# Optimization experiments

Hardware: AMD Instinct MI355X
Metric: run time of the kernel (lower is better)

The kernel has to match this reference:

```python
import jax, jax.numpy as jnp
import numpy as np

N, E = 10000, 320000
IN_CH, HID, OUT_CH, HEADS = 128, 64, 40, 8
NEG_SLOPE = 0.2


def gat_conv(x, src, dst, W, a_src, a_dst, bias, heads, C, concat, n_nodes):
    # x: [N, F_in]; W: [F_in, heads*C]; a_src/a_dst: [heads, C]
    h = (x @ W).reshape(n_nodes, heads, C)              # [N,H,C]
    alpha_src = jnp.sum(h * a_src, axis=-1)             # [N,H]
    alpha_dst = jnp.sum(h * a_dst, axis=-1)             # [N,H]
    score = jax.nn.leaky_relu(alpha_src[src] + alpha_dst[dst], NEG_SLOPE)  # [E,H]
    # segment softmax over edges sharing the same destination node
    smax = jax.ops.segment_max(score, dst, num_segments=n_nodes)
    smax = jnp.where(jnp.isfinite(smax), smax, 0.0)
    ex = jnp.exp(score - smax[dst])
    denom = jax.ops.segment_sum(ex, dst, num_segments=n_nodes)
    alpha = ex / (denom[dst] + 1e-16)                   # [E,H]
    msg = h[src] * alpha[:, :, None]                    # [E,H,C]
    out = jax.ops.segment_sum(msg, dst, num_segments=n_nodes)  # [N,H,C]
    out = out.reshape(n_nodes, heads * C) if concat else out.mean(axis=1)
    return out + bias


def setup_inputs() -> dict:
    key = jax.random.key(0)
    ks = jax.random.split(key, 16)
    g = 0.1
    return {
        "x": jax.random.normal(ks[0], (N, IN_CH), jnp.float32),
        "edge_index": jax.random.randint(ks[1], (2, E), 0, N, jnp.int64),
        "W1": jax.random.normal(ks[2], (IN_CH, HID), jnp.float32) * g,
        "b1": jnp.zeros((HID,), jnp.float32),
        "Wc1": jax.random.normal(ks[3], (HID, HEADS * HID), jnp.float32) * g,
        "att_src1": jax.random.normal(ks[4], (HEADS, HID), jnp.float32) * g,
        "att_dst1": jax.random.normal(ks[5], (HEADS, HID), jnp.float32) * g,
        "bc1": jnp.zeros((HEADS * HID,), jnp.float32),
        "Wc2": jax.random.normal(ks[6], (HEADS * HID, HID), jnp.float32) * g,
        "att_src2": jax.random.normal(ks[7], (1, HID), jnp.float32) * g,
        "att_dst2": jax.random.normal(ks[8], (1, HID), jnp.float32) * g,
        "bc2": jnp.zeros((HID,), jnp.float32),
        "W2": jax.random.normal(ks[9], (HID, OUT_CH), jnp.float32) * g,
        "b2": jnp.zeros((OUT_CH,), jnp.float32),
    }


def reference(x, edge_index, W1, b1, Wc1, att_src1, att_dst1, bc1,
              Wc2, att_src2, att_dst2, bc2, W2, b2):
    # add self-loops (PyG GATConv default add_self_loops=True)
    loop = jnp.arange(N, dtype=edge_index.dtype)
    src = jnp.concatenate([edge_index[0], loop])
    dst = jnp.concatenate([edge_index[1], loop])

    h = jax.nn.relu(x @ W1 + b1)                                   # lin0 + relu (dropout off in eval)
    h = jax.nn.elu(gat_conv(h, src, dst, Wc1, att_src1, att_dst1, bc1,
                            HEADS, HID, True, N))                  # conv1, concat heads
    h = gat_conv(h, src, dst, Wc2, att_src2, att_dst2, bc2,
                 1, HID, False, N)                                 # conv2, single head
    return h @ W2 + b2
```

## Files before the change

### kernel.cpp

```cpp
#include <hip/hip_runtime.h>
#include <cstdint>
#include <cstddef>

#define IN_CH 128
#define HID 64
#define HEADS 8
#define OUT_CH 40
#define NEG 0.2f
#define PAD 128
#define KP 136

typedef __attribute__((ext_vector_type(8))) short bf16x8;
typedef __attribute__((ext_vector_type(4))) float f32x4;

#define MFMA(a, b, c) __builtin_amdgcn_mfma_f32_16x16x32_bf16(a, b, c, 0, 0, 0)

__device__ inline unsigned short f2bf(float f) {
    unsigned u = __float_as_uint(f);
    unsigned r = (u + 0x7FFFu + ((u >> 16) & 1u)) >> 16;
    return (unsigned short)r;
}
__device__ inline float bf2f(unsigned short b) {
    return __uint_as_float((unsigned)b << 16);
}
__device__ inline bf16x8 ldb8(const unsigned short* p) {
    return *reinterpret_cast<const bf16x8*>(p);
}


__global__ void k_init(const float* __restrict__ W1,
                       const float* __restrict__ Wc1, const float* __restrict__ Wc2,
                       const float* __restrict__ as1, const float* __restrict__ ad1,
                       int* __restrict__ cursor,
                       unsigned short* __restrict__ W1T,
                       unsigned short* __restrict__ Wc1T, unsigned short* __restrict__ Wc2T,
                       unsigned short* __restrict__ vaT, int N) {
    int i = blockIdx.x * 256 + threadIdx.x;
    if (i < N) { cursor[i] = 0; return; }
    i -= N;
    if (i < 64 * 128) {
        int j = i >> 7, k = i & 127;
        W1T[i] = f2bf(W1[k * 64 + j]);
        return;
    }
    i -= 64 * 128;
    if (i < 512 * 64) {
        int j = i >> 6, k = i & 63;
        Wc1T[i] = f2bf(Wc1[(size_t)k * 512 + j]);
        return;
    }
    i -= 512 * 64;
    if (i < 64 * 512) {
        int j = i >> 9, k = i & 511;
        Wc2T[i] = f2bf(Wc2[(size_t)k * 64 + j]);
        return;
    }
    i -= 64 * 512;
    if (i < 8192) {
        int u = i >> 3, q = i & 7;
        int t = u >> 6, k = u & 63;
        int h = t & 7;
        const float* a = (t < 8) ? as1 : ad1;
        float sum = 0.f;
#pragma unroll
        for (int c2 = q * 8; c2 < q * 8 + 8; ++c2)
            sum += Wc1[(size_t)k * 512 + h * 64 + c2] * a[h * 64 + c2];
        sum += __shfl_xor(sum, 1);
        sum += __shfl_xor(sum, 2);
        sum += __shfl_xor(sum, 4);
        if (q == 0) vaT[t * 64 + k] = f2bf(sum);
    }
}


__global__ __launch_bounds__(256) void k_lin1m(const float* __restrict__ x,
                                               const unsigned short* __restrict__ W1T,
                                               const float* __restrict__ b1,
                                               const unsigned short* __restrict__ vaT,
                                               unsigned short* __restrict__ h0b,
                                               float* __restrict__ asrc, float* __restrict__ adst,
                                               const int* __restrict__ ei, int E, int T,
                                               int* __restrict__ cursor, int* __restrict__ csrc,
                                               int N, int NB) {
    __shared__ unsigned short h0s[16][72];
    if (blockIdx.x >= NB) {
        int e = (blockIdx.x - NB) * 256 + threadIdx.x;
        if (e < T) {
            int s, d;
            if (e < E) { s = ei[e]; d = ei[E + e]; } else { s = d = e - E; }
            int pos = atomicAdd(&cursor[d], 1);
            csrc[(size_t)d * PAD + pos] = s;
        }
        return;
    }
    int w = threadIdx.x >> 6, l = threadIdx.x & 63;
    int m0 = blockIdx.x * 16;
    int c = l & 15, g = l >> 4;
    int xr = m0 + c; if (xr >= N) xr = N - 1;
    bf16x8 af[4];
    const float* arow = x + (size_t)xr * 128 + 8 * g;
#pragma unroll
    for (int ks = 0; ks < 4; ++ks) {
        float4 f0 = *(const float4*)(arow + 32 * ks);
        float4 f1 = *(const float4*)(arow + 32 * ks + 4);
        bf16x8 t;
        t[0] = (short)f2bf(f0.x); t[1] = (short)f2bf(f0.y);
        t[2] = (short)f2bf(f0.z); t[3] = (short)f2bf(f0.w);
        t[4] = (short)f2bf(f1.x); t[5] = (short)f2bf(f1.y);
        t[6] = (short)f2bf(f1.z); t[7] = (short)f2bf(f1.w);
        af[ks] = t;
    }
    const unsigned short* brow = W1T + (size_t)(16 * w + c) * 128 + 8 * g;
    f32x4 acca = {}, accb = {};
    acca = MFMA(af[0], ldb8(brow), acca);
    accb = MFMA(af[1], ldb8(brow + 32), accb);
    acca = MFMA(af[2], ldb8(brow + 64), acca);
    accb = MFMA(af[3], ldb8(brow + 96), accb);
    f32x4 acc = acca + accb;
    int j = 16 * w + c;
    float bj = b1[j];
#pragma unroll
    for (int r = 0; r < 4; ++r) {
        float v = fmaxf(acc[r] + bj, 0.f);
        unsigned short us = f2bf(v);
        int row = m0 + 4 * g + r;
        if (row < N) h0b[(size_t)row * 64 + j] = us;
        h0s[4 * g + r][j] = us;
    }
    __syncthreads();
    if (w == 0) {
        bf16x8 a0 = ldb8(&h0s[c][8 * g]);
        bf16x8 a1 = ldb8(&h0s[c][32 + 8 * g]);
        bf16x8 b0 = ldb8(&vaT[c * 64 + 8 * g]);
        bf16x8 b1v = ldb8(&vaT[c * 64 + 32 + 8 * g]);
        f32x4 al = {};
        al = MFMA(a0, b0, al);
        al = MFMA(a1, b1v, al);
#pragma unroll
        for (int r = 0; r < 4; ++r) {
            int n = m0 + 4 * g + r;
            if (n < N) {
                if (c < 8) asrc[n * 8 + c] = al[r];
                else       adst[n * 8 + (c - 8)] = al[r];
            }
        }
    }
}


__global__ __launch_bounds__(128) void k_conv1agg(const unsigned short* __restrict__ h0b,
                                                  const float* __restrict__ asrc, const float* __restrict__ adst,
                                                  const int* __restrict__ degs, const int* __restrict__ csrc,
                                                  unsigned short* __restrict__ aggb, int N) {
    __shared__ int srcb[PAD];
    __shared__ float mx[8], den[8], adl[8];
    __shared__ unsigned short wA[16][KP];
    __shared__ unsigned short BT[64][KP];
    float (*sbf)[8] = (float(*)[8]) & BT[0][0];
    int tid = threadIdx.x;
    int n = blockIdx.x;
    int deg = degs[n];
    int K32 = (deg + 31) & ~31;
    if (tid < 8) adl[tid] = adst[n * 8 + tid];
    __syncthreads();
    if (tid < deg) {
        int s = csrc[(size_t)n * PAD + tid];
        srcb[tid] = s;
        const float4* ap = (const float4*)&asrc[(size_t)s * 8];
        float4 a0 = ap[0], a1 = ap[1];
        float v;
        float4 s0, s1;
        v = a0.x + adl[0]; s0.x = (v >= 0.f) ? v : NEG * v;
        v = a0.y + adl[1]; s0.y = (v >= 0.f) ? v : NEG * v;
        v = a0.z + adl[2]; s0.z = (v >= 0.f) ? v : NEG * v;
        v = a0.w + adl[3]; s0.w = (v >= 0.f) ? v : NEG * v;
        v = a1.x + adl[4]; s1.x = (v >= 0.f) ? v : NEG * v;
        v = a1.y + adl[5]; s1.y = (v >= 0.f) ? v : NEG * v;
        v = a1.z + adl[6]; s1.z = (v >= 0.f) ? v : NEG * v;
        v = a1.w + adl[7]; s1.w = (v >= 0.f) ? v : NEG * v;
        *(float4*)&sbf[tid][0] = s0;
        *(float4*)&sbf[tid][4] = s1;
    }
    __syncthreads();
    if (tid < 64) {
        int hh = tid & 7, idx = tid >> 3;
        float m = -1e30f;
        for (int i = idx; i < deg; i += 8) m = fmaxf(m, sbf[i][hh]);
        m = fmaxf(m, __shfl_xor(m, 8));
        m = fmaxf(m, __shfl_xor(m, 16));
        m = fmaxf(m, __shfl_xor(m, 32));
        if (tid < 8) mx[tid] = m;
    }
    __syncthreads();
    if (tid < 64) {
        int hh = tid & 7, idx = tid >> 3;
        float mh = mx[hh];
        float d = 0.f;
        for (int i = idx; i < K32; i += 8) {
            float ev = 0.f;
            if (i < deg) { ev = __expf(sbf[i][hh] - mh); d += ev; }
            wA[hh][i] = f2bf(ev);
        }
        d += __shfl_xor(d, 8);
        d += __shfl_xor(d, 16);
        d += __shfl_xor(d, 32);
        if (tid < 8) den[tid] = d + 1e-16f;
    }
    __syncthreads();
    for (int idx = tid; idx < K32 * 32; idx += 128) {
        int e = idx >> 5, cp = idx & 31;
        unsigned u = 0;
        if (e < deg) u = *(const unsigned*)&h0b[(size_t)srcb[e] * 64 + 2 * cp];
        BT[2 * cp][e] = (unsigned short)(u & 0xFFFFu);
        BT[2 * cp + 1][e] = (unsigned short)(u >> 16);
    }
    __syncthreads();
    int w = tid >> 6, l = tid & 63;
    int c = l & 15, g = l >> 4;
    f32x4 acc0 = {}, acc1 = {};
    for (int ks = 0; ks < (K32 >> 5); ++ks) {
        bf16x8 af = ldb8(&wA[c][32 * ks + 8 * g]);
        acc0 = MFMA(af, ldb8(&BT[32 * w + c][32 * ks + 8 * g]), acc0);
        acc1 = MFMA(af, ldb8(&BT[32 * w + 16 + c][32 * ks + 8 * g]), acc1);
    }
    if (g < 2) {
#pragma unroll
        for (int r = 0; r < 4; ++r) {
            int h = 4 * g + r;
            float dh = den[h];
            aggb[(size_t)n * 512 + h * 64 + 32 * w + c]      = f2bf(acc0[r] / dh);
            aggb[(size_t)n * 512 + h * 64 + 32 * w + 16 + c] = f2bf(acc1[r] / dh);
        }
    }
}


__global__ __launch_bounds__(256) void k_p1l2(const unsigned short* __restrict__ aggb,
                                              const unsigned short* __restrict__ Wc1T,
                                              const float* __restrict__ bc1,
                                              const unsigned short* __restrict__ Wc2T,
                                              const float* __restrict__ as2, const float* __restrict__ ad2,
                                              unsigned short* __restrict__ hc2b,
                                              float* __restrict__ asrc, float* __restrict__ adst, int N) {
    __shared__ unsigned short h1s[16][520];
    __shared__ float pps[4][16][2];
    int w = threadIdx.x >> 6, l = threadIdx.x & 63;
    int m0 = blockIdx.x * 16;
    int c = l & 15, g = l >> 4;
#pragma unroll
    for (int hl = 0; hl < 2; ++hl) {
        int h = 2 * w + hl;
        const unsigned short* arow = aggb + (size_t)(m0 + c) * 512 + h * 64 + 8 * g;
        bf16x8 af0 = ldb8(arow), af1 = ldb8(arow + 32);
        f32x4 acc[4] = {};
#pragma unroll
        for (int nt = 0; nt < 4; ++nt) {
            const unsigned short* brow = Wc1T + (size_t)(h * 64 + 16 * nt + c) * 64 + 8 * g;
            acc[nt] = MFMA(af0, ldb8(brow), acc[nt]);
            acc[nt] = MFMA(af1, ldb8(brow + 32), acc[nt]);
        }
#pragma unroll
        for (int nt = 0; nt < 4; ++nt) {
            int j = h * 64 + 16 * nt + c;
            float bj = bc1[j];
#pragma unroll
            for (int r = 0; r < 4; ++r) {
                float v = acc[nt][r] + bj;
                v = (v > 0.f) ? v : __expf(v) - 1.f;
                h1s[4 * g + r][j] = f2bf(v);
            }
        }
    }
    __syncthreads();
    const unsigned short* brow2 = Wc2T + (size_t)(16 * w + c) * 512 + 8 * g;
    f32x4 acc2a = {}, acc2b = {};
#pragma unroll
    for (int ks = 0; ks < 8; ++ks) {
        acc2a = MFMA(ldb8(&h1s[c][32 * ks + 8 * g]), ldb8(brow2 + 32 * ks), acc2a);
        acc2b = MFMA(ldb8(&h1s[c][32 * (ks + 8) + 8 * g]), ldb8(brow2 + 32 * (ks + 8)), acc2b);
    }
    f32x4 acc2 = acc2a + acc2b;
    int j = 16 * w + c;
    float aj = as2[j], dj = ad2[j];
    float ps[4], pd[4];
#pragma unroll
    for (int r = 0; r < 4; ++r) {
        float v = acc2[r];
        hc2b[(size_t)(m0 + 4 * g + r) * 64 + j] = f2bf(v);
        ps[r] = v * aj;
        pd[r] = v * dj;
    }
#pragma unroll
    for (int r = 0; r < 4; ++r) {
        float s = ps[r], d = pd[r];
        s += __shfl_xor(s, 1); s += __shfl_xor(s, 2); s += __shfl_xor(s, 4); s += __shfl_xor(s, 8);
        d += __shfl_xor(d, 1); d += __shfl_xor(d, 2); d += __shfl_xor(d, 4); d += __shfl_xor(d, 8);
        if (c == 0) {
            pps[w][4 * g + r][0] = s;
            pps[w][4 * g + r][1] = d;
        }
    }
    __syncthreads();
    int tid = threadIdx.x;
    if (tid < 32) {
        int row = tid >> 1, sel = tid & 1;
        float sum = pps[0][row][sel] + pps[1][row][sel] + pps[2][row][sel] + pps[3][row][sel];
        int n = m0 + row;
        if (n < N) {
            if (sel == 0) asrc[n] = sum;
            else          adst[n] = sum;
        }
    }
}


__global__ __launch_bounds__(256) void k_conv2f(const unsigned short* __restrict__ hc2b,
                                                const float* __restrict__ asrc, const float* __restrict__ adst,
                                                const int* __restrict__ degs, const int* __restrict__ csrc,
                                                const float* __restrict__ bc2,
                                                const float* __restrict__ W2, const float* __restrict__ b2,
                                                float* __restrict__ out, int N) {
    __shared__ float w2s[HID * OUT_CH];
    __shared__ float cosh_[4][HID];
    int tid = threadIdx.x;
    for (int i = tid; i < HID * OUT_CH; i += 256) w2s[i] = W2[i];
    int lane = tid & 63, nl = tid >> 6;
    int half = lane >> 5, cl = lane & 31;
    int n = blockIdx.x * 4 + nl;
    if (n < N) {
        int deg = degs[n];
        float ad = adst[n];
        float rm = -1e30f, rden = 0.f;
        float ax = 0.f, ay = 0.f;
        for (int base = 0; base < deg; base += 64) {
            int cnt = min(64, deg - base);
            int s = 0;
            float sc = -1e30f;
            if (lane < cnt) {
                s = csrc[(size_t)n * PAD + base + lane];
                float v = asrc[s] + ad;
                sc = (v >= 0.f) ? v : NEG * v;
            }
            float m = sc;
#pragma unroll
            for (int mm = 1; mm < 64; mm <<= 1) m = fmaxf(m, __shfl_xor(m, mm));
            float nmv = fmaxf(rm, m);
            float scale = __expf(rm - nmv);
            float p = (lane < cnt) ? __expf(sc - nmv) : 0.f;
            float d = p;
#pragma unroll
            for (int mm = 1; mm < 64; mm <<= 1) d += __shfl_xor(d, mm);
            rden = rden * scale + d;
            rm = nmv;
            ax *= scale; ay *= scale;
            for (int i = 0; i < cnt; i += 2) {
                int idx = i + half;
                float pi = __shfl(p, idx);
                int si = __shfl(s, idx);
                unsigned uu = *(const unsigned*)&hc2b[(size_t)si * 64 + 2 * cl];
                ax += pi * bf2f((unsigned short)(uu & 0xFFFFu));
                ay += pi * bf2f((unsigned short)(uu >> 16));
            }
        }
        ax += __shfl_xor(ax, 32);
        ay += __shfl_xor(ay, 32);
        if (half == 0) {
            float inv = 1.f / (rden + 1e-16f);
            cosh_[nl][2 * cl] = ax * inv + bc2[2 * cl];
            cosh_[nl][2 * cl + 1] = ay * inv + bc2[2 * cl + 1];
        }
    }
    __syncthreads();
    if (tid >= 160) return;
    int nn = tid / 40, j = tid % 40;
    int no = blockIdx.x * 4 + nn;
    if (no >= N) return;
    float s = b2[j];
#pragma unroll 8
    for (int k = 0; k < HID; ++k) s += cosh_[nn][k] * w2s[k * OUT_CH + j];
    out[(size_t)no * OUT_CH + j] = s;
}


extern "C" void kernel_launch(void* const* d_in, const int* in_sizes, int n_in,
                              void* d_out, int out_size, void* d_ws, size_t ws_size,
                              hipStream_t stream) {
    const float* x   = (const float*)d_in[0];
    const int*   ei  = (const int*)d_in[1];
    const float* W1  = (const float*)d_in[2];
    const float* b1  = (const float*)d_in[3];
    const float* Wc1 = (const float*)d_in[4];
    const float* as1 = (const float*)d_in[5];
    const float* ad1 = (const float*)d_in[6];
    const float* bc1 = (const float*)d_in[7];
    const float* Wc2 = (const float*)d_in[8];
    const float* as2 = (const float*)d_in[9];
    const float* ad2 = (const float*)d_in[10];
    const float* bc2 = (const float*)d_in[11];
    const float* W2  = (const float*)d_in[12];
    const float* b2  = (const float*)d_in[13];

    const int N = in_sizes[0] / IN_CH;
    const int E = in_sizes[1] / 2;
    const int T = E + N;

    char* base = (char*)d_ws;
    size_t off = 0;
    auto carve = [&](size_t bytes) -> void* {
        off = (off + 255) & ~(size_t)255;
        void* r = base + off;
        off += bytes;
        return r;
    };
    int* cursor     = (int*)carve((size_t)N * 4);
    int* csrc       = (int*)carve((size_t)N * PAD * 4);
    unsigned short* W1T  = (unsigned short*)carve((size_t)64 * 128 * 2);
    unsigned short* Wc1T = (unsigned short*)carve((size_t)512 * 64 * 2);
    unsigned short* Wc2T = (unsigned short*)carve((size_t)64 * 512 * 2);
    unsigned short* vaT  = (unsigned short*)carve((size_t)16 * 64 * 2);
    unsigned short* h0b  = (unsigned short*)carve((size_t)N * 64 * 2);
    float* asrc1    = (float*)carve((size_t)N * 8 * 4);
    float* adst1    = (float*)carve((size_t)N * 8 * 4);
    unsigned short* aggb = (unsigned short*)carve((size_t)N * 512 * 2);
    unsigned short* hc2b = (unsigned short*)carve((size_t)N * 64 * 2);
    float* asrc2    = (float*)carve((size_t)N * 4);
    float* adst2    = (float*)carve((size_t)N * 4);

    int init_total = N + 64 * 128 + 512 * 64 + 64 * 512 + 8192;
    k_init<<<(init_total + 255) / 256, 256, 0, stream>>>(W1, Wc1, Wc2, as1, ad1, cursor,
                                                         W1T, Wc1T, Wc2T, vaT, N);

    int NB = (N + 15) / 16;
    int FB = (T + 255) / 256;
    k_lin1m<<<NB + FB, 256, 0, stream>>>(x, W1T, b1, vaT, h0b, asrc1, adst1,
                                         ei, E, T, cursor, csrc, N, NB);
    k_conv1agg<<<N, 128, 0, stream>>>(h0b, asrc1, adst1, cursor, csrc, aggb, N);
    k_p1l2<<<(N + 15) / 16, 256, 0, stream>>>(aggb, Wc1T, bc1, Wc2T, as2, ad2,
                                              hc2b, asrc2, adst2, N);
    k_conv2f<<<(N + 3) / 4, 256, 0, stream>>>(hc2b, asrc2, adst2, cursor, csrc, bc2, W2, b2,
                                              (float*)d_out, N);
}
```

Before: 111.5 us.

## Rewrite conv1 aggregation as one wavefront per node with online softmax

The conv1 aggregation kernel now assigns one 64-lane wavefront per destination node, eight nodes per 512-thread block, instead of one 128-thread block per node. It replaces the block-wide barriers and the MFMA over a transposed LDS tile with wave-local syncs and scalar FMA accumulation, and uses an online (running max and rescale) softmax over 64-edge chunks. The aim is to cut barrier overhead, per-block launch cost and LDS transpose traffic, and to raise occupancy. In exchange it gives up MFMA throughput, relies on wave-level memory ordering, and issues per-edge 16-bit gathers for each lane.

```diff
diff --git a/kernel.cpp b/kernel.cpp
--- a/kernel.cpp
+++ b/kernel.cpp
@@ -8,7 +8,6 @@
 #define OUT_CH 40
 #define NEG 0.2f
 #define PAD 128
-#define KP 136
 
 typedef __attribute__((ext_vector_type(8))) short bf16x8;
 typedef __attribute__((ext_vector_type(4))) float f32x4;
@@ -25,6 +24,11 @@
 }
 __device__ inline bf16x8 ldb8(const unsigned short* p) {
     return *reinterpret_cast<const bf16x8*>(p);
+}
+__device__ __forceinline__ void wsync() {
+    __builtin_amdgcn_wave_barrier();
+    __threadfence_block();
+    __builtin_amdgcn_wave_barrier();
 }
 
 
@@ -148,90 +152,93 @@
 }
 
 
-__global__ __launch_bounds__(128) void k_conv1agg(const unsigned short* __restrict__ h0b,
+__global__ __launch_bounds__(512) void k_conv1agg(const unsigned short* __restrict__ h0b,
                                                   const float* __restrict__ asrc, const float* __restrict__ adst,
                                                   const int* __restrict__ degs, const int* __restrict__ csrc,
                                                   unsigned short* __restrict__ aggb, int N) {
-    __shared__ int srcb[PAD];
-    __shared__ float mx[8], den[8], adl[8];
-    __shared__ unsigned short wA[16][KP];
-    __shared__ unsigned short BT[64][KP];
-    float (*sbf)[8] = (float(*)[8]) & BT[0][0];
-    int tid = threadIdx.x;
-    int n = blockIdx.x;
+    __shared__ float sbw[8][64][8];
+    __shared__ int srcw[8][64];
+    __shared__ float scl[8][8];
+    __shared__ float dnw[8][8];
+    int w = threadIdx.x >> 6, l = threadIdx.x & 63;
+    int n = blockIdx.x * 8 + w;
+    if (n >= N) return;
     int deg = degs[n];
-    int K32 = (deg + 31) & ~31;
-    if (tid < 8) adl[tid] = adst[n * 8 + tid];
-    __syncthreads();
-    if (tid < deg) {
-        int s = csrc[(size_t)n * PAD + tid];
-        srcb[tid] = s;
-        const float4* ap = (const float4*)&asrc[(size_t)s * 8];
-        float4 a0 = ap[0], a1 = ap[1];
-        float v;
-        float4 s0, s1;
-        v = a0.x + adl[0]; s0.x = (v >= 0.f) ? v : NEG * v;
-        v = a0.y + adl[1]; s0.y = (v >= 0.f) ? v : NEG * v;
-        v = a0.z + adl[2]; s0.z = (v >= 0.f) ? v : NEG * v;
-        v = a0.w + adl[3]; s0.w = (v >= 0.f) ? v : NEG * v;
-        v = a1.x + adl[4]; s1.x = (v >= 0.f) ? v : NEG * v;
-        v = a1.y + adl[5]; s1.y = (v >= 0.f) ? v : NEG * v;
-        v = a1.z + adl[6]; s1.z = (v >= 0.f) ? v : NEG * v;
-        v = a1.w + adl[7]; s1.w = (v >= 0.f) ? v : NEG * v;
-        *(float4*)&sbf[tid][0] = s0;
-        *(float4*)&sbf[tid][4] = s1;
-    }
-    __syncthreads();
-    if (tid < 64) {
-        int hh = tid & 7, idx = tid >> 3;
+    float4 ad0 = *(const float4*)&adst[(size_t)n * 8];
+    float4 ad1 = *(const float4*)&adst[(size_t)n * 8 + 4];
+    int hh = l & 7, idx = l >> 3;
+    float rm = -1e30f, rden = 0.f;
+    float acc[8] = {0.f, 0.f, 0.f, 0.f, 0.f, 0.f, 0.f, 0.f};
+    for (int base = 0; base < deg; base += 64) {
+        int cnt = min(64, deg - base);
+        wsync();
+        if (l < cnt) {
+            int s = csrc[(size_t)n * PAD + base + l];
+            srcw[w][l] = s;
+            float4 a0 = *(const float4*)&asrc[(size_t)s * 8];
+            float4 a1 = *(const float4*)&asrc[(size_t)s * 8 + 4];
+            float v;
+            float4 s0, s1;
+            v = a0.x + ad0.x; s0.x = (v >= 0.f) ? v : NEG * v;
+            v = a0.y + ad0.y; s0.y = (v >= 0.f) ? v : NEG * v;
+            v = a0.z + ad0.z; s0.z = (v >= 0.f) ? v : NEG * v;
+            v = a0.w + ad0.w; s0.w = (v >= 0.f) ? v : NEG * v;
+            v = a1.x + ad1.x; s1.x = (v >= 0.f) ? v : NEG * v;
+            v = a1.y + ad1.y; s1.y = (v >= 0.f) ? v : NEG * v;
+            v = a1.z + ad1.z; s1.z = (v >= 0.f) ? v : NEG * v;
+            v = a1.w + ad1.w; s1.w = (v >= 0.f) ? v : NEG * v;
+            *(float4*)&sbw[w][l][0] = s0;
+            *(float4*)&sbw[w][l][4] = s1;
+        }
+        wsync();
         float m = -1e30f;
-        for (int i = idx; i < deg; i += 8) m = fmaxf(m, sbf[i][hh]);
+        for (int i = idx; i < cnt; i += 8) m = fmaxf(m, sbw[w][i][hh]);
         m = fmaxf(m, __shfl_xor(m, 8));
         m = fmaxf(m, __shfl_xor(m, 16));
         m = fmaxf(m, __shfl_xor(m, 32));
-        if (tid < 8) mx[tid] = m;
-    }
-    __syncthreads();
-    if (tid < 64) {
-        int hh = tid & 7, idx = tid >> 3;
-        float mh = mx[hh];
+        float nm = fmaxf(rm, m);
+        float sc = __expf(rm - nm);
+        rm = nm;
+        if (l < 8) scl[w][l] = sc;
         float d = 0.f;
-        for (int i = idx; i < K32; i += 8) {
-            float ev = 0.f;
-            if (i < deg) { ev = __expf(sbf[i][hh] - mh); d += ev; }
-            wA[hh][i] = f2bf(ev);
+        for (int i = idx; i < cnt; i += 8) {
+            float e = __expf(sbw[w][i][hh] - nm);
+            sbw[w][i][hh] = e;
+            d += e;
         }
         d += __shfl_xor(d, 8);
         d += __shfl_xor(d, 16);
         d += __shfl_xor(d, 32);
-        if (tid < 8) den[tid] = d + 1e-16f;
-    }
-    __syncthreads();
-    for (int idx = tid; idx < K32 * 32; idx += 128) {
-        int e = idx >> 5, cp = idx & 31;
-        unsigned u = 0;
-        if (e < deg) u = *(const unsigned*)&h0b[(size_t)srcb[e] * 64 + 2 * cp];
-        BT[2 * cp][e] = (unsigned short)(u & 0xFFFFu);
-        BT[2 * cp + 1][e] = (unsigned short)(u >> 16);
-    }
-    __syncthreads();
-    int w = tid >> 6, l = tid & 63;
-    int c = l & 15, g = l >> 4;
-    f32x4 acc0 = {}, acc1 = {};
-    for (int ks = 0; ks < (K32 >> 5); ++ks) {
-        bf16x8 af = ldb8(&wA[c][32 * ks + 8 * g]);
-        acc0 = MFMA(af, ldb8(&BT[32 * w + c][32 * ks + 8 * g]), acc0);
-        acc1 = MFMA(af, ldb8(&BT[32 * w + 16 + c][32 * ks + 8 * g]), acc1);
-    }
-    if (g < 2) {
-#pragma unroll
-        for (int r = 0; r < 4; ++r) {
-            int h = 4 * g + r;
-            float dh = den[h];
-            aggb[(size_t)n * 512 + h * 64 + 32 * w + c]      = f2bf(acc0[r] / dh);
-            aggb[(size_t)n * 512 + h * 64 + 32 * w + 16 + c] = f2bf(acc1[r] / dh);
-        }
-    }
+        rden = rden * sc + d;
+        wsync();
+        float4 sc0 = *(const float4*)&scl[w][0];
+        float4 sc1 = *(const float4*)&scl[w][4];
+        acc[0] *= sc0.x; acc[1] *= sc0.y; acc[2] *= sc0.z; acc[3] *= sc0.w;
+        acc[4] *= sc1.x; acc[5] *= sc1.y; acc[6] *= sc1.z; acc[7] *= sc1.w;
+        for (int e = 0; e < cnt; ++e) {
+            int s = srcw[w][e];
+            float v = bf2f(h0b[(size_t)s * 64 + l]);
+            float4 w0 = *(const float4*)&sbw[w][e][0];
+            float4 w1 = *(const float4*)&sbw[w][e][4];
+            acc[0] += w0.x * v; acc[1] += w0.y * v;
+            acc[2] += w0.z * v; acc[3] += w0.w * v;
+            acc[4] += w1.x * v; acc[5] += w1.y * v;
+            acc[6] += w1.z * v; acc[7] += w1.w * v;
+        }
+    }
+    if (l < 8) dnw[w][l] = rden + 1e-16f;
+    wsync();
+    float4 d0 = *(const float4*)&dnw[w][0];
+    float4 d1 = *(const float4*)&dnw[w][4];
+    unsigned short* outp = aggb + (size_t)n * 512 + l;
+    outp[0]       = f2bf(acc[0] / d0.x);
+    outp[64]      = f2bf(acc[1] / d0.y);
+    outp[128]     = f2bf(acc[2] / d0.z);
+    outp[192]     = f2bf(acc[3] / d0.w);
+    outp[256]     = f2bf(acc[4] / d1.x);
+    outp[320]     = f2bf(acc[5] / d1.y);
+    outp[384]     = f2bf(acc[6] / d1.z);
+    outp[448]     = f2bf(acc[7] / d1.w);
 }
 
 
@@ -434,7 +441,7 @@
     int FB = (T + 255) / 256;
     k_lin1m<<<NB + FB, 256, 0, stream>>>(x, W1T, b1, vaT, h0b, asrc1, adst1,
                                          ei, E, T, cursor, csrc, N, NB);
-    k_conv1agg<<<N, 128, 0, stream>>>(h0b, asrc1, adst1, cursor, csrc, aggb, N);
+    k_conv1agg<<<(N + 7) / 8, 512, 0, stream>>>(h0b, asrc1, adst1, cursor, csrc, aggb, N);
     k_p1l2<<<(N + 15) / 16, 256, 0, stream>>>(aggb, Wc1T, bc1, Wc2T, as2, ad2,
                                               hc2b, asrc2, adst2, N);
     k_conv2f<<<(N + 3) / 4, 256, 0, stream>>>(hc2b, asrc2, adst2, cursor, csrc, bc2, W2, b2,
```

Measured after the change: 100.0 us. 10.3% less time.
